# Optimization experiments

Measured on AMD Instinct MI355X. Metric: run time of the kernel, lower is better.

The kernel has to match this reference:

```python
import jax, jax.numpy as jnp
import numpy as np

NUM_CODES = 1024
CODE_DIM = 64
EMA_DECAY = 0.99
COMMIT_W = 0.25
EPS = 1e-5
B = 262144


def setup_inputs() -> dict:
    key = jax.random.key(0)
    k1, k2, k3, k4 = jax.random.split(key, 4)
    z = jax.random.normal(k1, (B, CODE_DIM), dtype=jnp.float32)
    weight = jax.random.normal(k2, (NUM_CODES, CODE_DIM), dtype=jnp.float32)
    ema_cluster_size = jax.random.uniform(k3, (NUM_CODES,), dtype=jnp.float32)
    ema_embed_sum = jax.random.normal(k4, (NUM_CODES, CODE_DIM), dtype=jnp.float32)
    return {"z": z, "weight": weight, "ema_cluster_size": ema_cluster_size,
            "ema_embed_sum": ema_embed_sum}


def reference(z, weight, ema_cluster_size, ema_embed_sum):
    # Squared Euclidean distances (argmin equivalent to cdist argmin)
    # d2[b,k] = ||z_b||^2 - 2 z_b . w_k + ||w_k||^2
    z2 = jnp.sum(z * z, axis=-1, keepdims=True)          # (B, 1)
    w2 = jnp.sum(weight * weight, axis=-1)               # (K,)
    d2 = z2 - 2.0 * (z @ weight.T) + w2[None, :]         # (B, K)
    indices = jnp.argmin(d2, axis=-1)                    # (B,)
    z_q = weight[indices]                                # gather with OLD weights

    # EMA codebook update (training, ema_update=True)
    ones = jnp.ones((z.shape[0],), dtype=z.dtype)
    cluster_size = jax.ops.segment_sum(ones, indices, num_segments=NUM_CODES)
    embed_sum = jax.ops.segment_sum(z, indices, num_segments=NUM_CODES)
    new_cs = EMA_DECAY * ema_cluster_size + (1.0 - EMA_DECAY) * cluster_size
    new_es = EMA_DECAY * ema_embed_sum + (1.0 - EMA_DECAY) * embed_sum
    n = jnp.sum(new_cs)
    smoothed = (new_cs + EPS) / (n + NUM_CODES * EPS) * n
    new_weight = new_es / smoothed[:, None]

    # commitment loss (z detached in torch; pure value here)
    vq_loss = COMMIT_W * jnp.mean((z - z_q) ** 2)

    # straight-through estimator
    z_q_st = z + jax.lax.stop_gradient(z_q - z)
    return z_q_st, indices, vq_loss, new_cs, new_es, new_weight
```

## Files before the change

kernel.cpp:

```cpp
#include <hip/hip_runtime.h>

typedef __attribute__((ext_vector_type(8))) short bf16x8;
typedef __attribute__((ext_vector_type(4))) float f32x4;

#define B_ROWS 262144
#define K_CODES 1024
#define DIM 64
#define SDELTA 0.015f

#define OUT_ZQ 0
#define OUT_IDX 16777216
#define OUT_LOSS 17039360
#define OUT_NEWCS 17039361
#define OUT_NEWES 17040385
#define OUT_NEWW 17105921

#define WS_LOSS   0
#define WS_QCOUNT 1
#define WS_W2     16
#define WS_SMOOTH 1040
#define WS_WHIP   2064
#define WS_WLOP   34832
#define WS_CPART  67600
#define WS_EPART  100368
#define WS_MINI   2197520
#define WS_QUEUE  2459664

static __device__ __forceinline__ unsigned short f2bf(float x) {
    unsigned u = __float_as_uint(x);
    return (unsigned short)((u + 0x7fffu + ((u >> 16) & 1u)) >> 16);
}
static __device__ __forceinline__ float bf2f(unsigned short u) {
    return __uint_as_float(((unsigned)u) << 16);
}

static __device__ __forceinline__ float red16(float x) {
    int v;
    v = __builtin_amdgcn_update_dpp(0, __float_as_int(x), 0x128, 0xF, 0xF, true);
    x += __int_as_float(v);
    v = __builtin_amdgcn_update_dpp(0, __float_as_int(x), 0x124, 0xF, 0xF, true);
    x += __int_as_float(v);
    v = __builtin_amdgcn_update_dpp(0, __float_as_int(x), 0x122, 0xF, 0xF, true);
    x += __int_as_float(v);
    v = __builtin_amdgcn_update_dpp(0, __float_as_int(x), 0x121, 0xF, 0xF, true);
    x += __int_as_float(v);
    return x;
}

static __device__ __forceinline__ void cvt_frag(const float* zrow, bf16x8& hi, bf16x8& lo) {
    float4 f0 = *(const float4*)zrow;
    float4 f1 = *(const float4*)(zrow + 4);
    float tf[8] = {f0.x, f0.y, f0.z, f0.w, f1.x, f1.y, f1.z, f1.w};
#pragma unroll
    for (int j = 0; j < 8; ++j) {
        unsigned short h = f2bf(tf[j]);
        hi[j] = (short)h;
        lo[j] = (short)f2bf(tf[j] - bf2f(h));
    }
}

__global__ __launch_bounds__(256) void vq_prep(const float* __restrict__ w,
                                               float* __restrict__ ws) {
    int b = blockIdx.x, tid = threadIdx.x;
    if (b < 4) {
        int k = b * 256 + tid;
        const float4* w4 = (const float4*)(w + (size_t)k * DIM);
        float s = 0.f;
#pragma unroll
        for (int j = 0; j < 16; ++j) {
            float4 v = w4[j];
            s += v.x * v.x + v.y * v.y + v.z * v.z + v.w * v.w;
        }
        ws[WS_W2 + k] = s;
    } else {
        int i = (b - 4) * 256 + tid;
        int p = i & 1023, c = i >> 10;
        int code = c * 128 + ((p >> 7) << 4) + (p & 15);
        int octet = ((p >> 6) & 1) * 4 + ((p >> 4) & 3);
        const float* src = w + (size_t)code * DIM + octet * 8;
        float4 f0 = *(const float4*)src;
        float4 f1 = *(const float4*)(src + 4);
        float tf[8] = {f0.x, f0.y, f0.z, f0.w, f1.x, f1.y, f1.z, f1.w};
        bf16x8 hv, lv;
#pragma unroll
        for (int j = 0; j < 8; ++j) {
            unsigned short hb = f2bf(tf[j]);
            hv[j] = (short)hb;
            lv[j] = (short)f2bf(tf[j] - bf2f(hb));
        }
        ((bf16x8*)(ws + WS_WHIP))[i] = hv;
        ((bf16x8*)(ws + WS_WLOP))[i] = lv;
    }
}

__global__ __launch_bounds__(256)
__attribute__((amdgpu_waves_per_eu(3, 4))) void vq_screen_kernel(
    const float* __restrict__ z, float* __restrict__ ws) {
    __shared__ float lds_w2h[K_CODES];

    int tid = threadIdx.x;
    int l = tid & 63, wave = tid >> 6;
    int m = l & 15, q = l >> 4;

    {
        float4 wv = ((const float4*)(ws + WS_W2))[tid];
        float4 hv;
        hv.x = -0.5f * wv.x;
        hv.y = -0.5f * wv.y;
        hv.z = -0.5f * wv.z;
        hv.w = -0.5f * wv.w;
        *(float4*)&lds_w2h[tid * 4] = hv;
    }

    int rowbase = blockIdx.x * 128 + wave * 32;
    bf16x8 zhi[2][2], zlo[2][2];
#pragma unroll
    for (int g = 0; g < 2; ++g) {
        const float* zr = z + (size_t)(rowbase + g * 16 + m) * DIM + q * 8;
        cvt_frag(zr, zhi[g][0], zlo[g][0]);
        cvt_frag(zr + 32, zhi[g][1], zlo[g][1]);
    }

    float kv[2], k2[2];
    kv[0] = kv[1] = -3.4e38f;
    k2[0] = k2[1] = -3.4e38f;

    const bf16x8* __restrict__ gh = (const bf16x8*)(ws + WS_WHIP);
    const bf16x8* __restrict__ gl = (const bf16x8*)(ws + WS_WLOP);

    __syncthreads();

    for (int cch = 0; cch < 8; ++cch) {
#pragma unroll 2
        for (int tg = 0; tg < 8; ++tg) {
            int gi = cch * 1024 + tg * 128 + l;
            bf16x8 bh0 = gh[gi];
            bf16x8 bh1 = gh[gi + 64];
            bf16x8 bl0 = gl[gi];
            bf16x8 bl1 = gl[gi + 64];
            unsigned cbase = (unsigned)(cch * 128 + tg * 16 + q * 4);
            unsigned ibase = (unsigned)((cch * 8 + tg) * 4);
            f32x4 cinit = *(const f32x4*)&lds_w2h[cbase];
#pragma unroll
            for (int g = 0; g < 2; ++g) {
                f32x4 acc = cinit;
                acc = __builtin_amdgcn_mfma_f32_16x16x32_bf16(bh0, zlo[g][0], acc, 0, 0, 0);
                acc = __builtin_amdgcn_mfma_f32_16x16x32_bf16(bl0, zhi[g][0], acc, 0, 0, 0);
                acc = __builtin_amdgcn_mfma_f32_16x16x32_bf16(bh1, zlo[g][1], acc, 0, 0, 0);
                acc = __builtin_amdgcn_mfma_f32_16x16x32_bf16(bl1, zhi[g][1], acc, 0, 0, 0);
                acc = __builtin_amdgcn_mfma_f32_16x16x32_bf16(bh0, zhi[g][0], acc, 0, 0, 0);
                acc = __builtin_amdgcn_mfma_f32_16x16x32_bf16(bh1, zhi[g][1], acc, 0, 0, 0);
                float a0 = __uint_as_float((__float_as_uint(acc[0]) & 0xFFFFFF00u) | ibase);
                float a1 = __uint_as_float((__float_as_uint(acc[1]) & 0xFFFFFF00u) | (ibase + 1u));
                float a2 = __uint_as_float((__float_as_uint(acc[2]) & 0xFFFFFF00u) | (ibase + 2u));
                float a3 = __uint_as_float((__float_as_uint(acc[3]) & 0xFFFFFF00u) | (ibase + 3u));
                float m01 = fmaxf(a0, a1), n01 = fminf(a0, a1);
                float m23 = fmaxf(a2, a3), n23 = fminf(a2, a3);
                float top = fmaxf(m01, m23);
                float sec = fmaxf(fmaxf(fminf(m01, m23), n01), n23);
                k2[g] = fmaxf(fmaxf(k2[g], sec), fminf(kv[g], top));
                kv[g] = fmaxf(kv[g], top);
            }
        }
    }

    float mv[2], m2[2];
    int mi[2];
#pragma unroll
    for (int g = 0; g < 2; ++g) {
        unsigned kb = __float_as_uint(kv[g]);
        unsigned i8 = kb & 255u;
        mi[g] = (int)((i8 >> 5) * 128 + ((i8 >> 2) & 7) * 16 + (unsigned)q * 4 + (i8 & 3));
        mv[g] = __uint_as_float(kb & 0xFFFFFF00u);
        m2[g] = __uint_as_float(__float_as_uint(k2[g]) & 0xFFFFFF00u);
    }
#pragma unroll
    for (int o = 16; o < 64; o <<= 1) {
#pragma unroll
        for (int g = 0; g < 2; ++g) {
            float ov = __shfl_xor(mv[g], o, 64);
            float ov2 = __shfl_xor(m2[g], o, 64);
            int oi = __shfl_xor(mi[g], o, 64);
            float nm2 = fmaxf(fmaxf(m2[g], ov2), fminf(mv[g], ov));
            bool take = (ov > mv[g]) || (ov == mv[g] && oi < mi[g]);
            mv[g] = take ? ov : mv[g];
            mi[g] = take ? oi : mi[g];
            m2[g] = nm2;
        }
    }
    if (q == 0) {
#pragma unroll
        for (int g = 0; g < 2; ++g) {
            bool amb = (mv[g] - m2[g]) <= SDELTA;
            ((int*)ws)[WS_MINI + rowbase + g * 16 + m] = mi[g] | (amb ? 0x80000000 : 0);
        }
    }
}

__global__ __launch_bounds__(256) void vq_gather_kernel(
    const float* __restrict__ z, const float* __restrict__ w,
    float* __restrict__ ws, float* __restrict__ out) {
    __shared__ float lred[4];
    int tid = threadIdx.x;
    int lane = tid & 63, wave = tid >> 6;
    int rsub = lane >> 4;
    int d4 = lane & 15;
    int wavebase = blockIdx.x * 256 + wave * 64;

    int encv[16];
#pragma unroll
    for (int s = 0; s < 16; ++s)
        encv[s] = ((const int*)ws)[WS_MINI + wavebase + s * 4 + rsub];

    float lsum = 0.f;
#pragma unroll
    for (int s = 0; s < 16; ++s) {
        int row = wavebase + s * 4 + rsub;
        int enc = encv[s];
        if (enc >= 0) {
            float4 x = ((const float4*)(z + (size_t)row * DIM))[d4];
            float4 qv = ((const float4*)(w + (size_t)enc * DIM))[d4];
            float4 st;
            st.x = x.x + (qv.x - x.x);
            st.y = x.y + (qv.y - x.y);
            st.z = x.z + (qv.z - x.z);
            st.w = x.w + (qv.w - x.w);
            ((float4*)(out + OUT_ZQ + (size_t)row * DIM))[d4] = st;
            float e0 = x.x - qv.x, e1 = x.y - qv.y, e2 = x.z - qv.z, e3 = x.w - qv.w;
            lsum += e0 * e0;
            lsum += e1 * e1;
            lsum += e2 * e2;
            lsum += e3 * e3;
            if (d4 == 0) out[OUT_IDX + row] = (float)enc;
        } else if (d4 == 0) {
            int pos = atomicAdd((int*)ws + WS_QCOUNT, 1);
            ((int*)ws)[WS_QUEUE + pos] = row;
        }
    }
#pragma unroll
    for (int o = 32; o; o >>= 1) lsum += __shfl_down(lsum, o, 64);
    if (lane == 0) lred[wave] = lsum;
    __syncthreads();
    if (tid == 0) atomicAdd(ws + WS_LOSS, lred[0] + lred[1] + lred[2] + lred[3]);
}

__global__ __launch_bounds__(256) void vq_fixup_kernel(
    const float* __restrict__ z, const float* __restrict__ w,
    float* __restrict__ ws, float* __restrict__ out) {
    const float* __restrict__ w2 = ws + WS_W2;
    __shared__ float sdd[4][4];
    __shared__ int sbi[4][4];
    int count = ((const int*)ws)[WS_QCOUNT];
    int tid = threadIdx.x;
    int lane = tid & 63, wave = tid >> 6;
    int sub = lane >> 4, d4 = lane & 15;
    float lacc = 0.f;
    for (int q0 = blockIdx.x * 4; q0 < count; q0 += gridDim.x * 4) {
        int qi = q0 + sub;
        bool active = qi < count;
        int row = ((const int*)ws)[WS_QUEUE + (active ? qi : 0)];
        float4 zx = ((const float4*)(z + (size_t)row * DIM))[d4];
        float zp = zx.x * zx.x;
        zp = fmaf(zx.y, zx.y, zp);
        zp = fmaf(zx.z, zx.z, zp);
        zp = fmaf(zx.w, zx.w, zp);
        float z2 = red16(zp);
        float best = 3.4e38f;
        int bi = 0;
        int c0 = wave * 256;
#pragma unroll 4
        for (int cc = 0; cc < 256; ++cc) {
            int c = c0 + cc;
            float4 wv4 = ((const float4*)(w + (size_t)c * DIM))[d4];
            float p = zx.x * wv4.x;
            p = fmaf(zx.y, wv4.y, p);
            p = fmaf(zx.z, wv4.z, p);
            p = fmaf(zx.w, wv4.w, p);
            p = red16(p);
            float dd = (z2 - 2.f * p) + w2[c];
            if (dd < best) { best = dd; bi = c; }
        }
        if (d4 == 0) { sdd[wave][sub] = best; sbi[wave][sub] = bi; }
        __syncthreads();
        if (wave == 0 && active) {
            float fb = sdd[0][sub];
            int fbi = sbi[0][sub];
#pragma unroll
            for (int v = 1; v < 4; ++v) {
                float od = sdd[v][sub];
                int oi = sbi[v][sub];
                if (od < fb || (od == fb && oi < fbi)) { fb = od; fbi = oi; }
            }
            float4 qv = ((const float4*)(w + (size_t)fbi * DIM))[d4];
            float4 st;
            st.x = zx.x + (qv.x - zx.x);
            st.y = zx.y + (qv.y - zx.y);
            st.z = zx.z + (qv.z - zx.z);
            st.w = zx.w + (qv.w - zx.w);
            ((float4*)(out + OUT_ZQ + (size_t)row * DIM))[d4] = st;
            float e0 = zx.x - qv.x, e1 = zx.y - qv.y;
            float e2 = zx.z - qv.z, e3 = zx.w - qv.w;
            float ls = e0 * e0 + e1 * e1 + e2 * e2 + e3 * e3;
            ls = red16(ls);
            if (d4 == 0) {
                out[OUT_IDX + row] = (float)fbi;
                lacc += ls;
            }
        }
        __syncthreads();
    }
    lacc += __shfl_xor(lacc, 16, 64);
    lacc += __shfl_xor(lacc, 32, 64);
    if (tid == 0 && lacc != 0.f) atomicAdd(ws + WS_LOSS, lacc);
}

__global__ __launch_bounds__(1024) void vq_embed_kernel(
    const float* __restrict__ z, const float* __restrict__ idx_f,
    float* __restrict__ ws) {
    __shared__ float eacc[K_CODES * 16];
    __shared__ float scnt[K_CODES];
    int b = blockIdx.x;
    int rs = b >> 2, q = b & 3;
    int tid = threadIdx.x;
    int lane = tid & 63, wave = tid >> 6;
    int sub = lane >> 4, d = lane & 15;

#pragma unroll
    for (int j = 0; j < 16; ++j) eacc[j * 1024 + tid] = 0.f;
    if (tid < 1024) scnt[tid] = 0.f;
    __syncthreads();

    int rbase = rs * 8192 + wave * 512 + sub;
    const float* zq = z + q * 16 + d;
#pragma unroll 4
    for (int i = 0; i < 128; ++i) {
        int row = rbase + i * 4;
        float cf = idx_f[row];
        float zv = zq[(size_t)row * DIM];
        int code = (int)cf;
        atomicAdd(&eacc[code * 16 + d], zv);
        if (q == 0 && d == 0) atomicAdd(&scnt[code], 1.f);
    }
    __syncthreads();
#pragma unroll
    for (int j = 0; j < 16; ++j)
        ws[WS_EPART + ((size_t)b * 16384) + j * 1024 + tid] = eacc[j * 1024 + tid];
    if (q == 0) ws[WS_CPART + rs * 1024 + tid] = scnt[tid];
}

__global__ __launch_bounds__(1024) void vq_finalize1_kernel(
    const float* __restrict__ ema_cs, float* __restrict__ ws,
    float* __restrict__ out) {
    int k = threadIdx.x;
    float c = 0.f;
#pragma unroll
    for (int rs = 0; rs < 32; ++rs) c += ws[WS_CPART + rs * 1024 + k];
    float nc = 0.99f * ema_cs[k] + 0.01f * c;
    out[OUT_NEWCS + k] = nc;

    float s = nc;
#pragma unroll
    for (int o = 32; o; o >>= 1) s += __shfl_down(s, o, 64);
    __shared__ float red[16];
    __shared__ float n_sh;
    if ((k & 63) == 0) red[k >> 6] = s;
    __syncthreads();
    if (k == 0) {
        float n = 0.f;
#pragma unroll
        for (int i = 0; i < 16; ++i) n += red[i];
        n_sh = n;
        out[OUT_LOSS] = 0.25f * (ws[WS_LOSS] / 16777216.0f);
    }
    __syncthreads();
    float n = n_sh;
    ws[WS_SMOOTH + k] = (nc + 1e-5f) / (n + 0.01024f) * n;
}

__global__ __launch_bounds__(256) void vq_finalize2_kernel(
    const float* __restrict__ ema_es, const float* __restrict__ ws,
    float* __restrict__ out) {
    int i = blockIdx.x * 256 + threadIdx.x;
    int code = i >> 6, dim = i & 63;
    int q = dim >> 4, d16 = dim & 15;
    float e = 0.f;
#pragma unroll
    for (int rs = 0; rs < 32; ++rs)
        e += ws[WS_EPART + (size_t)(rs * 4 + q) * 16384 + code * 16 + d16];
    float es = 0.99f * ema_es[i] + 0.01f * e;
    out[OUT_NEWES + i] = es;
    out[OUT_NEWW + i] = es / ws[WS_SMOOTH + code];
}

extern "C" void kernel_launch(void* const* d_in, const int* in_sizes, int n_in,
                              void* d_out, int out_size, void* d_ws, size_t ws_size,
                              hipStream_t stream) {
    const float* z = (const float*)d_in[0];
    const float* weight = (const float*)d_in[1];
    const float* ema_cs = (const float*)d_in[2];
    const float* ema_es = (const float*)d_in[3];
    float* out = (float*)d_out;
    float* ws = (float*)d_ws;

    hipMemsetAsync(ws, 0, 64, stream);
    vq_prep<<<36, 256, 0, stream>>>(weight, ws);
    vq_screen_kernel<<<B_ROWS / 128, 256, 0, stream>>>(z, ws);
    vq_gather_kernel<<<B_ROWS / 256, 256, 0, stream>>>(z, weight, ws, out);
    vq_fixup_kernel<<<512, 256, 0, stream>>>(z, weight, ws, out);
    vq_embed_kernel<<<128, 1024, 0, stream>>>(z, out + OUT_IDX, ws);
    vq_finalize1_kernel<<<1, 1024, 0, stream>>>(ema_cs, ws, out);
    vq_finalize2_kernel<<<256, 256, 0, stream>>>(ema_es, ws, out);
}
```

Before: 452.8 us.

## Replace LDS-histogram embed sum with replicated global atomic accumulation

The segment-sum kernel now spreads rows over 2048 small blocks. Each block does float4 loads of z rows and global atomicAdds into one of 8 replicated accumulator copies, instead of 128 large blocks that each build a 16-dim-slice histogram in shared memory and write it out in full. The finalize kernels now sum 8 replicas instead of 32 partials, and two memsets zero the replicas. This aims to fix the low occupancy and large partial write and read traffic, at the cost of heavy global atomic contention on hot codes.

```diff
diff --git a/kernel.cpp b/kernel.cpp
--- a/kernel.cpp
+++ b/kernel.cpp
@@ -7,6 +7,7 @@
 #define K_CODES 1024
 #define DIM 64
 #define SDELTA 0.015f
+#define NREP 8
 
 #define OUT_ZQ 0
 #define OUT_IDX 16777216
@@ -314,38 +315,29 @@
     if (tid == 0 && lacc != 0.f) atomicAdd(ws + WS_LOSS, lacc);
 }
 
-__global__ __launch_bounds__(1024) void vq_embed_kernel(
+__global__ __launch_bounds__(256) void vq_embed_kernel(
     const float* __restrict__ z, const float* __restrict__ idx_f,
     float* __restrict__ ws) {
-    __shared__ float eacc[K_CODES * 16];
-    __shared__ float scnt[K_CODES];
-    int b = blockIdx.x;
-    int rs = b >> 2, q = b & 3;
     int tid = threadIdx.x;
     int lane = tid & 63, wave = tid >> 6;
-    int sub = lane >> 4, d = lane & 15;
-
-#pragma unroll
-    for (int j = 0; j < 16; ++j) eacc[j * 1024 + tid] = 0.f;
-    if (tid < 1024) scnt[tid] = 0.f;
-    __syncthreads();
-
-    int rbase = rs * 8192 + wave * 512 + sub;
-    const float* zq = z + q * 16 + d;
-#pragma unroll 4
-    for (int i = 0; i < 128; ++i) {
-        int row = rbase + i * 4;
+    int sub = lane >> 4, d4 = lane & 15;
+    int rep = blockIdx.x & (NREP - 1);
+    float* __restrict__ eacc = ws + WS_EPART + rep * (K_CODES * DIM);
+    float* __restrict__ cacc = ws + WS_CPART + rep * K_CODES;
+    int base = blockIdx.x * 128 + wave * 4 + sub;
+#pragma unroll 2
+    for (int it = 0; it < 8; ++it) {
+        int row = base + it * 16;
         float cf = idx_f[row];
-        float zv = zq[(size_t)row * DIM];
+        float4 zv = ((const float4*)(z + (size_t)row * DIM))[d4];
         int code = (int)cf;
-        atomicAdd(&eacc[code * 16 + d], zv);
-        if (q == 0 && d == 0) atomicAdd(&scnt[code], 1.f);
-    }
-    __syncthreads();
-#pragma unroll
-    for (int j = 0; j < 16; ++j)
-        ws[WS_EPART + ((size_t)b * 16384) + j * 1024 + tid] = eacc[j * 1024 + tid];
-    if (q == 0) ws[WS_CPART + rs * 1024 + tid] = scnt[tid];
+        float* dst = eacc + code * DIM + d4 * 4;
+        atomicAdd(dst + 0, zv.x);
+        atomicAdd(dst + 1, zv.y);
+        atomicAdd(dst + 2, zv.z);
+        atomicAdd(dst + 3, zv.w);
+        if (d4 == 0) atomicAdd(cacc + code, 1.f);
+    }
 }
 
 __global__ __launch_bounds__(1024) void vq_finalize1_kernel(
@@ -354,7 +346,7 @@
     int k = threadIdx.x;
     float c = 0.f;
 #pragma unroll
-    for (int rs = 0; rs < 32; ++rs) c += ws[WS_CPART + rs * 1024 + k];
+    for (int r = 0; r < NREP; ++r) c += ws[WS_CPART + r * K_CODES + k];
     float nc = 0.99f * ema_cs[k] + 0.01f * c;
     out[OUT_NEWCS + k] = nc;
 
@@ -381,12 +373,10 @@
     const float* __restrict__ ema_es, const float* __restrict__ ws,
     float* __restrict__ out) {
     int i = blockIdx.x * 256 + threadIdx.x;
-    int code = i >> 6, dim = i & 63;
-    int q = dim >> 4, d16 = dim & 15;
+    int code = i >> 6;
     float e = 0.f;
 #pragma unroll
-    for (int rs = 0; rs < 32; ++rs)
-        e += ws[WS_EPART + (size_t)(rs * 4 + q) * 16384 + code * 16 + d16];
+    for (int r = 0; r < NREP; ++r) e += ws[WS_EPART + r * (K_CODES * DIM) + i];
     float es = 0.99f * ema_es[i] + 0.01f * e;
     out[OUT_NEWES + i] = es;
     out[OUT_NEWW + i] = es / ws[WS_SMOOTH + code];
@@ -403,11 +393,13 @@
     float* ws = (float*)d_ws;
 
     hipMemsetAsync(ws, 0, 64, stream);
+    hipMemsetAsync(ws + WS_CPART, 0, NREP * K_CODES * 4, stream);
+    hipMemsetAsync(ws + WS_EPART, 0, NREP * K_CODES * DIM * 4, stream);
     vq_prep<<<36, 256, 0, stream>>>(weight, ws);
     vq_screen_kernel<<<B_ROWS / 128, 256, 0, stream>>>(z, ws);
     vq_gather_kernel<<<B_ROWS / 256, 256, 0, stream>>>(z, weight, ws, out);
     vq_fixup_kernel<<<512, 256, 0, stream>>>(z, weight, ws, out);
-    vq_embed_kernel<<<128, 1024, 0, stream>>>(z, out + OUT_IDX, ws);
+    vq_embed_kernel<<<B_ROWS / 128, 256, 0, stream>>>(z, out + OUT_IDX, ws);
     vq_finalize1_kernel<<<1, 1024, 0, stream>>>(ema_cs, ws, out);
     vq_finalize2_kernel<<<256, 256, 0, stream>>>(ema_es, ws, out);
 }
```

Result: slower. 605.6 us (+33.7%).
